# Kernel tuning notes

Hardware: AMD Instinct MI355X
Metric: run time of the kernel (lower is better)

The kernel has to match this reference:

```python
import jax, jax.numpy as jnp
import numpy as np

N_OSC = 256
N_LAYERS = 4
STEPS = 10
DT = 0.1
B = 1024
D_IN = 512
D_OUT = 128


def setup_inputs() -> dict:
    key = jax.random.key(0)
    ks = jax.random.split(key, 12)
    n = N_OSC

    def rn(k, shape, s=1.0):
        return jax.random.normal(k, shape, jnp.float32) * s

    K = rn(ks[0], (N_LAYERS, n, n), 0.1)
    K = (K + jnp.swapaxes(K, -1, -2)) / 2  # symmetric init as in torch
    return {
        "x": rn(ks[1], (B, D_IN)),
        "enc_W1": rn(ks[2], (D_IN, 2 * n), 0.02), "enc_b1": jnp.zeros((2 * n,), jnp.float32),
        "enc_W2": rn(ks[3], (2 * n, n), 0.02), "enc_b2": jnp.zeros((n,), jnp.float32),
        "K": K,
        "omega": rn(ks[4], (N_LAYERS, n), 0.1),
        "K_global": jnp.full((N_LAYERS,), 0.5, jnp.float32),
        "op_strength": jnp.full((6,), 0.5, jnp.float32),
        "exchange_logits": rn(ks[5], (n, n), 0.1),
        "catalyze_freq": rn(ks[6], (n,), 0.1),
        "sel_W1": rn(ks[7], (n + 2, 64), 0.05), "sel_b1": jnp.zeros((64,), jnp.float32),
        "sel_W2": rn(ks[8], (64, 6), 0.05), "sel_b2": jnp.zeros((6,), jnp.float32),
        "dec_W1": rn(ks[9], (2 * n, 2 * D_OUT), 0.02), "dec_b1": jnp.zeros((2 * D_OUT,), jnp.float32),
        "dec_W2": rn(ks[10], (2 * D_OUT, D_OUT), 0.02), "dec_b2": jnp.zeros((D_OUT,), jnp.float32),
        "z_momentum": jnp.float32(0.1),
        "z_decay": jnp.float32(0.05),
    }


def _kuramoto_layer(theta, K, omega, K_global):
    n = theta.shape[-1]

    def step(th, _):
        diff = th[:, None, :] - th[:, :, None]          # [B, i, j] = theta_j - theta_i
        coupling = jnp.sum(K * jnp.sin(diff), axis=-1)  # reduce over j -> [B, n]
        th_new = th + DT * (omega + (K_global / n) * coupling)
        th_new = jnp.arctan2(jnp.sin(th_new), jnp.cos(th_new))  # wrap to (-pi, pi]
        return th_new, None

    theta, _ = jax.lax.scan(jax.checkpoint(step), theta, None, length=STEPS)
    cm = jnp.mean(jnp.cos(theta), axis=-1)
    sm = jnp.mean(jnp.sin(theta), axis=-1)
    return theta, jnp.sqrt(cm * cm + sm * sm)  # Kuramoto order parameter r


def _soft_permutation(logits):
    P = logits
    for _ in range(5):  # Sinkhorn normalization in log space
        P = P - jax.nn.logsumexp(P, axis=-1, keepdims=True)
        P = P - jax.nn.logsumexp(P, axis=-2, keepdims=True)
    return jnp.exp(P)


def _forward(x, enc_W1, enc_b1, enc_W2, enc_b2, K, omega, K_global,
             op_strength, exchange_logits, catalyze_freq,
             sel_W1, sel_b1, sel_W2, sel_b2, dec_W1, dec_b1, dec_W2, dec_b2,
             z_momentum, z_decay):
    n = N_OSC
    # input encoding -> initial phases in (-pi, pi)
    h = jax.nn.gelu(x @ enc_W1 + enc_b1, approximate=False)
    theta = jnp.tanh(h @ enc_W2 + enc_b2) * jnp.pi

    z = jnp.float32(0.1)
    P = _soft_permutation(exchange_logits)
    k_mult = jnp.float32(1.0)              # AMPLIFY/CONTAIN carry to next layer
    om_add = jnp.zeros((n,), theta.dtype)  # CATALYZE carry to next layer

    for li in range(N_LAYERS):
        theta, r = _kuramoto_layer(theta, K[li] * k_mult, omega[li] + om_add, K_global[li])
        # z-coordinate attractor update: dz = mom*(r_mean - z) - decay*(z - 0.5)
        dz = z_momentum * (jnp.mean(r) - z) - z_decay * (z - 0.5)
        z = jnp.clip(z + 0.01 * dz, 0.0, 1.0)
        # APL operator selection from [theta, coherence, z]
        feat = jnp.concatenate(
            [theta, r[:, None], jnp.broadcast_to(z, (theta.shape[0], 1))], axis=-1)
        logits = jax.nn.gelu(feat @ sel_W1 + sel_b1, approximate=False) @ sel_W2 + sel_b2
        op = jnp.argmax(jnp.mean(logits, axis=0))
        strength = op_strength[op] * r[:, None]  # coherence-modulated strength
        sm_ = jnp.mean(strength)
        # apply operator: phase mods now, K/omega mods carried into next layer
        noise = jax.random.normal(jax.random.fold_in(jax.random.key(42), li),
                                  theta.shape, theta.dtype)
        theta = jnp.where(op == 3, theta @ P,                                # EXCHANGE
                          jnp.where(op == 4, theta + noise * strength * 0.2,  # INHIBIT
                                    theta))
        k_mult = jnp.where(op == 1, 1.0 + sm_ * 0.5,        # AMPLIFY
                           jnp.where(op == 2, 1.0 - sm_ * 0.3, 1.0))  # CONTAIN
        om_add = jnp.where(op == 5, catalyze_freq * sm_,    # CATALYZE
                           jnp.zeros_like(catalyze_freq))

    # decode from (cos, sin) phase embedding
    emb = jnp.concatenate([jnp.cos(theta), jnp.sin(theta)], axis=-1)  # [B, 2n]
    out = jax.nn.gelu(emb @ dec_W1 + dec_b1, approximate=False) @ dec_W2 + dec_b2
    return out


def reference(x, enc_W1, enc_b1, enc_W2, enc_b2, K, omega, K_global,
              op_strength, exchange_logits, catalyze_freq,
              sel_W1, sel_b1, sel_W2, sel_b2, dec_W1, dec_b1, dec_W2, dec_b2,
              z_momentum, z_decay):
    return _forward(x, enc_W1, enc_b1, enc_W2, enc_b2, K, omega, K_global,
                    op_strength, exchange_logits, catalyze_freq,
                    sel_W1, sel_b1, sel_W2, sel_b2, dec_W1, dec_b1, dec_W2, dec_b2,
                    z_momentum, z_decay)
```

## Files before the change

kernel.cpp:

```cpp
#include <hip/hip_runtime.h>
#include <hip/hip_fp16.h>
#include <math.h>

#define DT_F 0.1f

#define SC_Z     0
#define SC_RMEAN 1
#define SC_KMULT 2
#define SC_OP    3
#define SC_OPSTR 4
#define SC_SM    5

typedef __attribute__((ext_vector_type(8))) short short8;
typedef __attribute__((ext_vector_type(4))) float f32x4;


__device__ __forceinline__ float gelu_f(float x) {
    return 0.5f * x * (1.0f + erff(x * 0.7071067811865475f));
}

__device__ __forceinline__ unsigned short f2bf_rne(float f) {
    union { float f; unsigned u; } v; v.f = f;
    unsigned x = v.u;
    unsigned r = x + 0x7fffu + ((x >> 16) & 1u);
    return (unsigned short)(r >> 16);
}

__device__ __forceinline__ unsigned rotl32(unsigned v, int d) {
    return (v << d) | (v >> (32 - d));
}

__device__ __forceinline__ void threefry2x32(unsigned k0, unsigned k1,
                                             unsigned x0, unsigned x1,
                                             unsigned& o0, unsigned& o1) {
    unsigned k2 = k0 ^ k1 ^ 0x1BD11BDAu;
    x0 += k0; x1 += k1;
    const int r0[4] = {13, 15, 26, 6};
    const int r1[4] = {17, 29, 16, 24};
#pragma unroll
    for (int g = 0; g < 5; ++g) {
        const int* R = (g & 1) ? r1 : r0;
#pragma unroll
        for (int q = 0; q < 4; ++q) { x0 += x1; x1 = rotl32(x1, R[q]); x1 ^= x0; }
        unsigned a, b;
        switch (g) {
            case 0:  a = k1; b = k2 + 1u; break;
            case 1:  a = k2; b = k0 + 2u; break;
            case 2:  a = k0; b = k1 + 3u; break;
            case 3:  a = k1; b = k2 + 4u; break;
            default: a = k2; b = k0 + 5u; break;
        }
        x0 += a; x1 += b;
    }
    o0 = x0; o1 = x1;
}

__device__ __forceinline__ float erfinv_xla(float x) {
    float w = -log1pf(-x * x);
    float p;
    if (w < 5.0f) {
        w -= 2.5f;
        p = 2.81022636e-08f;
        p = fmaf(p, w, 3.43273939e-07f);
        p = fmaf(p, w, -3.5233877e-06f);
        p = fmaf(p, w, -4.39150654e-06f);
        p = fmaf(p, w, 0.00021858087f);
        p = fmaf(p, w, -0.00125372503f);
        p = fmaf(p, w, -0.00417768164f);
        p = fmaf(p, w, 0.246640727f);
        p = fmaf(p, w, 1.50140941f);
    } else {
        w = sqrtf(w) - 3.0f;
        p = -0.000200214257f;
        p = fmaf(p, w, 0.000100950558f);
        p = fmaf(p, w, 0.00134934322f);
        p = fmaf(p, w, -0.00367342844f);
        p = fmaf(p, w, 0.00573950773f);
        p = fmaf(p, w, -0.0076224613f);
        p = fmaf(p, w, 0.00943887047f);
        p = fmaf(p, w, 1.00167406f);
        p = fmaf(p, w, 2.83297682f);
    }
    return p * x;
}

__device__ __forceinline__ float jax_normal_elem(unsigned fk0, unsigned fk1, unsigned flat) {
    const unsigned HALF = 131072u;
    unsigned idx = (flat < HALF) ? flat : (flat - HALF);
    unsigned o0, o1;
    threefry2x32(fk0, fk1, idx, idx + HALF, o0, o1);
    unsigned bits = (flat < HALF) ? o0 : o1;
    float f = __uint_as_float((bits >> 9) | 0x3F800000u) - 1.0f;
    const float LO = __uint_as_float(0xBF7FFFFFu);
    float u = fmaxf(LO, fmaf(f, 2.0f, LO));
    return 1.41421356237f * erfinv_xla(u);
}


__global__ __launch_bounds__(256) void prep_wt_kernel(
    const float* __restrict__ W1, const float* __restrict__ W2,
    const float* __restrict__ W3, const float* __restrict__ W4,
    unsigned short* __restrict__ T1, unsigned short* __restrict__ T2,
    unsigned short* __restrict__ T3, unsigned short* __restrict__ T4)
{
    __shared__ float tile[64][65];
    int b = blockIdx.x;
    const float* W; unsigned short* T; int K, N, kt, nt;
    if (b < 64)       { W = W1; T = T1; K = 512; N = 512; kt = b >> 3; nt = b & 7; }
    else if (b < 96)  { b -= 64;  W = W2; T = T2; K = 512; N = 256; kt = b >> 2; nt = b & 3; }
    else if (b < 128) { b -= 96;  W = W3; T = T3; K = 512; N = 256; kt = b >> 2; nt = b & 3; }
    else              { b -= 128; W = W4; T = T4; K = 256; N = 128; kt = b >> 1; nt = b & 1; }
    const int k0 = kt * 64, n0 = nt * 64;
    const int t = threadIdx.x;

#pragma unroll
    for (int i = 0; i < 4; ++i) {
        int r = (t >> 4) + i * 16;
        int c = (t & 15) * 4;
        float4 v = *reinterpret_cast<const float4*>(&W[(k0 + r) * N + n0 + c]);
        tile[r][c] = v.x; tile[r][c + 1] = v.y; tile[r][c + 2] = v.z; tile[r][c + 3] = v.w;
    }
    __syncthreads();
#pragma unroll
    for (int i = 0; i < 4; ++i) {
        int nn = (t >> 4) + i * 16;
        int kc = (t & 15) * 4;
        ushort4 o;
        o.x = f2bf_rne(tile[kc + 0][nn]);
        o.y = f2bf_rne(tile[kc + 1][nn]);
        o.z = f2bf_rne(tile[kc + 2][nn]);
        o.w = f2bf_rne(tile[kc + 3][nn]);
        *reinterpret_cast<ushort4*>(&T[(n0 + nn) * K + k0 + kc]) = o;
    }
}


template <int ACT, int KF, bool EMB>
__global__ __launch_bounds__(256) void gemm_mfma_kernel(
    const float* __restrict__ A,
    const unsigned short* __restrict__ Wt,
    const float* __restrict__ bias,
    float* __restrict__ C, int N)
{
    constexpr int STR = KF + 8;
    __shared__ __align__(16) unsigned short A_s[64 * STR];
    __shared__ __align__(16) unsigned short B_s[64 * STR];
    const int tid = threadIdx.x;
    const int m_base = blockIdx.y * 64;
    const int n_base = blockIdx.x * 64;

    {
        constexpr int ITERS = 64 * KF / 2048;
#pragma unroll
        for (int c = 0; c < ITERS; ++c) {
            const int f = c * 2048 + tid * 8;
            const int row = f / KF, k = f % KF;
            float4 a0, a1;
            if (EMB) {
                const int kk = k & 255;
                a0 = *reinterpret_cast<const float4*>(&A[(m_base + row) * 256 + kk]);
                a1 = *reinterpret_cast<const float4*>(&A[(m_base + row) * 256 + kk + 4]);
                if (k < 256) {
                    a0.x = __cosf(a0.x); a0.y = __cosf(a0.y); a0.z = __cosf(a0.z); a0.w = __cosf(a0.w);
                    a1.x = __cosf(a1.x); a1.y = __cosf(a1.y); a1.z = __cosf(a1.z); a1.w = __cosf(a1.w);
                } else {
                    a0.x = __sinf(a0.x); a0.y = __sinf(a0.y); a0.z = __sinf(a0.z); a0.w = __sinf(a0.w);
                    a1.x = __sinf(a1.x); a1.y = __sinf(a1.y); a1.z = __sinf(a1.z); a1.w = __sinf(a1.w);
                }
            } else {
                a0 = *reinterpret_cast<const float4*>(&A[(m_base + row) * KF + k]);
                a1 = *reinterpret_cast<const float4*>(&A[(m_base + row) * KF + k + 4]);
            }
            short8 v;
            v[0] = (short)f2bf_rne(a0.x); v[1] = (short)f2bf_rne(a0.y);
            v[2] = (short)f2bf_rne(a0.z); v[3] = (short)f2bf_rne(a0.w);
            v[4] = (short)f2bf_rne(a1.x); v[5] = (short)f2bf_rne(a1.y);
            v[6] = (short)f2bf_rne(a1.z); v[7] = (short)f2bf_rne(a1.w);
            *reinterpret_cast<short8*>(&A_s[row * STR + k]) = v;
        }
    }
    {
        constexpr int ITERS = 64 * KF / 2048;
#pragma unroll
        for (int c = 0; c < ITERS; ++c) {
            const int f = c * 2048 + tid * 8;
            const int n = f / KF, k = f % KF;
            short8 v = *reinterpret_cast<const short8*>(&Wt[(n_base + n) * KF + k]);
            *reinterpret_cast<short8*>(&B_s[n * STR + k]) = v;
        }
    }
    __syncthreads();

    const int l = tid & 63, w = tid >> 6;
    const int lo = l & 15, hi = l >> 4;

    f32x4 acc0 = {0.f, 0.f, 0.f, 0.f};
    f32x4 acc1 = {0.f, 0.f, 0.f, 0.f};
    f32x4 acc2 = {0.f, 0.f, 0.f, 0.f};
    f32x4 acc3 = {0.f, 0.f, 0.f, 0.f};
#pragma unroll
    for (int kc = 0; kc < KF / 32; ++kc) {
        short8 af = *reinterpret_cast<const short8*>(&A_s[(w * 16 + lo) * STR + kc * 32 + hi * 8]);
        short8 b0 = *reinterpret_cast<const short8*>(&B_s[(0 * 16 + lo) * STR + kc * 32 + hi * 8]);
        short8 b1 = *reinterpret_cast<const short8*>(&B_s[(1 * 16 + lo) * STR + kc * 32 + hi * 8]);
        short8 b2 = *reinterpret_cast<const short8*>(&B_s[(2 * 16 + lo) * STR + kc * 32 + hi * 8]);
        short8 b3 = *reinterpret_cast<const short8*>(&B_s[(3 * 16 + lo) * STR + kc * 32 + hi * 8]);
        acc0 = __builtin_amdgcn_mfma_f32_16x16x32_bf16(af, b0, acc0, 0, 0, 0);
        acc1 = __builtin_amdgcn_mfma_f32_16x16x32_bf16(af, b1, acc1, 0, 0, 0);
        acc2 = __builtin_amdgcn_mfma_f32_16x16x32_bf16(af, b2, acc2, 0, 0, 0);
        acc3 = __builtin_amdgcn_mfma_f32_16x16x32_bf16(af, b3, acc3, 0, 0, 0);
    }

#pragma unroll
    for (int nf = 0; nf < 4; ++nf) {
        const f32x4 a = (nf == 0) ? acc0 : (nf == 1) ? acc1 : (nf == 2) ? acc2 : acc3;
        const int n = n_base + nf * 16 + lo;
        const float bv = bias[n];
#pragma unroll
        for (int q = 0; q < 4; ++q) {
            const int m = m_base + w * 16 + hi * 4 + q;
            float v = a[q] + bv;
            if (ACT == 1) v = gelu_f(v);
            else if (ACT == 2) v = tanhf(v) * 3.14159274101257324f;
            C[m * N + n] = v;
        }
    }
}


__global__ __launch_bounds__(1024) void sinkhorn_kernel(const float* __restrict__ logits,
                                                        float* __restrict__ P,
                                                        float* __restrict__ scal,
                                                        float* __restrict__ om_add) {
    __shared__ __align__(16) __half Eh[256][260];
    __shared__ float a[256], b[256];
    __shared__ float part[8][256];
    const int t = threadIdx.x;

    if (t < 8) {
        float val = 0.0f;
        if (t == SC_Z) val = 0.1f;
        if (t == SC_KMULT) val = 1.0f;
        scal[t] = val;
    }
    if (t < 256) { om_add[t] = 0.0f; b[t] = 1.0f; }

    {
        const int r = t >> 2, c0 = (t & 3) * 64;
#pragma unroll
        for (int j = 0; j < 64; j += 4) {
            float4 x4 = *reinterpret_cast<const float4*>(&logits[r * 256 + c0 + j]);
            __half2 h01 = __floats2half2_rn(__expf(x4.x), __expf(x4.y));
            __half2 h23 = __floats2half2_rn(__expf(x4.z), __expf(x4.w));
            *reinterpret_cast<__half2*>(&Eh[r][c0 + j])     = h01;
            *reinterpret_cast<__half2*>(&Eh[r][c0 + j + 2]) = h23;
        }
    }
    __syncthreads();

    for (int it = 0; it < 5; ++it) {
        {
            const int i = t & 255, q = t >> 8;
            float s0 = 0.f, s1 = 0.f, s2 = 0.f, s3 = 0.f;
#pragma unroll
            for (int j0 = 0; j0 < 64; j0 += 4) {
                float2 e4 = *reinterpret_cast<const float2*>(&Eh[i][q * 64 + j0]);
                const __half2* hp = reinterpret_cast<const __half2*>(&e4);
                float2 f01 = __half22float2(hp[0]);
                float2 f23 = __half22float2(hp[1]);
                float4 bv = *reinterpret_cast<const float4*>(&b[q * 64 + j0]);
                s0 = fmaf(f01.x, bv.x, s0);
                s1 = fmaf(f01.y, bv.y, s1);
                s2 = fmaf(f23.x, bv.z, s2);
                s3 = fmaf(f23.y, bv.w, s3);
            }
            part[q][i] = (s0 + s1) + (s2 + s3);
        }
        __syncthreads();
        if (t < 256) a[t] = 1.0f / (part[0][t] + part[1][t] + part[2][t] + part[3][t]);
        __syncthreads();
        {
            const int jp = t & 127, seg = t >> 7;
            float s0 = 0.f, s1 = 0.f;
#pragma unroll
            for (int i0 = 0; i0 < 32; i0 += 4) {
                float4 av = *reinterpret_cast<const float4*>(&a[seg * 32 + i0]);
                __half2 e0 = *reinterpret_cast<const __half2*>(&Eh[seg * 32 + i0 + 0][2 * jp]);
                __half2 e1 = *reinterpret_cast<const __half2*>(&Eh[seg * 32 + i0 + 1][2 * jp]);
                __half2 e2 = *reinterpret_cast<const __half2*>(&Eh[seg * 32 + i0 + 2][2 * jp]);
                __half2 e3 = *reinterpret_cast<const __half2*>(&Eh[seg * 32 + i0 + 3][2 * jp]);
                float2 f0 = __half22float2(e0), f1 = __half22float2(e1);
                float2 f2 = __half22float2(e2), f3 = __half22float2(e3);
                s0 = fmaf(f0.x, av.x, s0); s1 = fmaf(f0.y, av.x, s1);
                s0 = fmaf(f1.x, av.y, s0); s1 = fmaf(f1.y, av.y, s1);
                s0 = fmaf(f2.x, av.z, s0); s1 = fmaf(f2.y, av.z, s1);
                s0 = fmaf(f3.x, av.w, s0); s1 = fmaf(f3.y, av.w, s1);
            }
            part[seg][2 * jp]     = s0;
            part[seg][2 * jp + 1] = s1;
        }
        __syncthreads();
        if (t < 256) {
            float s = ((part[0][t] + part[1][t]) + (part[2][t] + part[3][t]))
                    + ((part[4][t] + part[5][t]) + (part[6][t] + part[7][t]));
            b[t] = 1.0f / s;
        }
        __syncthreads();
    }

    {
        const int r = t >> 2, c0 = (t & 3) * 64;
        const float ar = a[r];
#pragma unroll
        for (int j = 0; j < 64; j += 4) {
            float2 e4 = *reinterpret_cast<const float2*>(&Eh[r][c0 + j]);
            const __half2* hp = reinterpret_cast<const __half2*>(&e4);
            float2 f01 = __half22float2(hp[0]);
            float2 f23 = __half22float2(hp[1]);
            float4 bv = *reinterpret_cast<const float4*>(&b[c0 + j]);
            float4 o;
            o.x = f01.x * ar * bv.x;
            o.y = f01.y * ar * bv.y;
            o.z = f23.x * ar * bv.z;
            o.w = f23.y * ar * bv.w;
            *reinterpret_cast<float4*>(&P[r * 256 + c0 + j]) = o;
        }
    }
}


__global__ __launch_bounds__(512) void kuramoto_mfma_kernel(
    float* __restrict__ theta,
    const float* __restrict__ Kl,
    const float* __restrict__ omega_l,
    const float* __restrict__ Kg_p,
    const float* __restrict__ scal,
    const float* __restrict__ om_add,
    float* __restrict__ r_out,
    float* __restrict__ rpart,
    const float* __restrict__ P,
    int li)
{
    __shared__ __align__(16) unsigned short s_lds[2][16][264];
    __shared__ __align__(16) unsigned short c_lds[2][16][264];
    __shared__ __align__(16) float th_lds[16][260];
    __shared__ float rp_s[16][128];
    __shared__ float rp_c[16][128];
    __shared__ float red_s[16][32];
    __shared__ float red_c[16][32];
    __shared__ float rloc[16];

    const int tid = threadIdx.x;
    const int l  = tid & 63;
    const int w  = tid >> 6;
    const int lo = l & 15;
    const int hi = l >> 4;
    const int cb = w * 32;
    const int r0 = blockIdx.x * 16;

    const float gk = Kg_p[0] * (1.0f / 256.0f) * scal[SC_KMULT];
    const int op_prev = (int)scal[SC_OP];

    {
        const int row = tid >> 5;
        const int c0 = (tid & 31) * 8;
        float4 a = *reinterpret_cast<const float4*>(&theta[(r0 + row) * 256 + c0]);
        float4 b = *reinterpret_cast<const float4*>(&theta[(r0 + row) * 256 + c0 + 4]);
        *reinterpret_cast<float4*>(&th_lds[row][c0])     = a;
        *reinterpret_cast<float4*>(&th_lds[row][c0 + 4]) = b;
    }

    short8 kfrag[8][2];
#pragma unroll
    for (int nf = 0; nf < 2; ++nf) {
        const int col = cb + nf * 16 + lo;
        const float* krow = Kl + col * 256;
#pragma unroll
        for (int ks = 0; ks < 8; ++ks) {
            const int kb = ks * 32 + hi * 8;
            float4 k0 = *reinterpret_cast<const float4*>(&krow[kb]);
            float4 k1 = *reinterpret_cast<const float4*>(&krow[kb + 4]);
            short8 f;
            f[0] = (short)f2bf_rne(k0.x); f[1] = (short)f2bf_rne(k0.y);
            f[2] = (short)f2bf_rne(k0.z); f[3] = (short)f2bf_rne(k0.w);
            f[4] = (short)f2bf_rne(k1.x); f[5] = (short)f2bf_rne(k1.y);
            f[6] = (short)f2bf_rne(k1.z); f[7] = (short)f2bf_rne(k1.w);
            kfrag[ks][nf] = f;
        }
    }
    __syncthreads();

    float t[2][4];
    if (op_prev == 3) {
        float acc[2][4] = {};
        for (int j = 0; j < 256; ++j) {
            float p0 = P[j * 256 + cb + lo];
            float p1 = P[j * 256 + cb + 16 + lo];
#pragma unroll
            for (int q = 0; q < 4; ++q) {
                float tv = th_lds[hi * 4 + q][j];
                acc[0][q] = fmaf(tv, p0, acc[0][q]);
                acc[1][q] = fmaf(tv, p1, acc[1][q]);
            }
        }
#pragma unroll
        for (int nf = 0; nf < 2; ++nf)
#pragma unroll
            for (int q = 0; q < 4; ++q) t[nf][q] = acc[nf][q];
    } else {
#pragma unroll
        for (int nf = 0; nf < 2; ++nf)
#pragma unroll
            for (int q = 0; q < 4; ++q)
                t[nf][q] = th_lds[hi * 4 + q][cb + nf * 16 + lo];
        if (op_prev == 4) {
            unsigned fk0, fk1;
            threefry2x32(0u, 42u, 0u, (unsigned)(li - 1), fk0, fk1);
            const float opv = scal[SC_OPSTR];
#pragma unroll
            for (int nf = 0; nf < 2; ++nf)
#pragma unroll
                for (int q = 0; q < 4; ++q) {
                    const int row = hi * 4 + q;
                    const int col = cb + nf * 16 + lo;
                    unsigned flat = (unsigned)((r0 + row) * 256 + col);
                    float nz = jax_normal_elem(fk0, fk1, flat);
                    t[nf][q] += nz * opv * r_out[r0 + row] * 0.2f;
                }
        }
    }

    float si[2][4], ci[2][4];
    float om[2];
#pragma unroll
    for (int nf = 0; nf < 2; ++nf) {
        const int col = cb + nf * 16 + lo;
        om[nf] = omega_l[col] + om_add[col];
#pragma unroll
        for (int q = 0; q < 4; ++q) {
            const int row = hi * 4 + q;
            float sv, cv;
            __sincosf(t[nf][q], &sv, &cv);
            si[nf][q] = sv; ci[nf][q] = cv;
            s_lds[0][row][col] = f2bf_rne(sv);
            c_lds[0][row][col] = f2bf_rne(cv);
        }
    }
    __syncthreads();

    int cur = 0;
    for (int s = 0; s < 10; ++s) {
        f32x4 accS0 = {0.f, 0.f, 0.f, 0.f};
        f32x4 accS1 = {0.f, 0.f, 0.f, 0.f};
        f32x4 accC0 = {0.f, 0.f, 0.f, 0.f};
        f32x4 accC1 = {0.f, 0.f, 0.f, 0.f};
#pragma unroll
        for (int ks = 0; ks < 8; ++ks) {
            short8 aS = *reinterpret_cast<const short8*>(&s_lds[cur][lo][ks * 32 + hi * 8]);
            short8 aC = *reinterpret_cast<const short8*>(&c_lds[cur][lo][ks * 32 + hi * 8]);
            accS0 = __builtin_amdgcn_mfma_f32_16x16x32_bf16(aS, kfrag[ks][0], accS0, 0, 0, 0);
            accS1 = __builtin_amdgcn_mfma_f32_16x16x32_bf16(aS, kfrag[ks][1], accS1, 0, 0, 0);
            accC0 = __builtin_amdgcn_mfma_f32_16x16x32_bf16(aC, kfrag[ks][0], accC0, 0, 0, 0);
            accC1 = __builtin_amdgcn_mfma_f32_16x16x32_bf16(aC, kfrag[ks][1], accC1, 0, 0, 0);
        }
        const int nxt = cur ^ 1;
#pragma unroll
        for (int nf = 0; nf < 2; ++nf) {
#pragma unroll
            for (int q = 0; q < 4; ++q) {
                float aS = (nf == 0) ? accS0[q] : accS1[q];
                float aC = (nf == 0) ? accC0[q] : accC1[q];
                float coup = ci[nf][q] * aS - si[nf][q] * aC;
                float tn = t[nf][q] + DT_F * (om[nf] + gk * coup);
                t[nf][q] = tn;
                float sv, cv;
                __sincosf(tn, &sv, &cv);
                si[nf][q] = sv; ci[nf][q] = cv;
                const int row = hi * 4 + q;
                const int col = cb + nf * 16 + lo;
                s_lds[nxt][row][col] = f2bf_rne(sv);
                c_lds[nxt][row][col] = f2bf_rne(cv);
            }
        }
        __syncthreads();
        cur = nxt;
    }

#pragma unroll
    for (int q = 0; q < 4; ++q) {
        const int row = hi * 4 + q;
        rp_s[row][w * 16 + lo] = si[0][q] + si[1][q];
        rp_c[row][w * 16 + lo] = ci[0][q] + ci[1][q];
    }
#pragma unroll
    for (int nf = 0; nf < 2; ++nf) {
#pragma unroll
        for (int q = 0; q < 4; ++q) {
            const int row = hi * 4 + q;
            const int col = cb + nf * 16 + lo;
            theta[(r0 + row) * 256 + col] = atan2f(si[nf][q], ci[nf][q]);
        }
    }
    __syncthreads();

    {
        const int row = tid >> 5;
        const int i = tid & 31;
        float ssum = rp_s[row][i] + rp_s[row][i + 32] + rp_s[row][i + 64] + rp_s[row][i + 96];
        float csum = rp_c[row][i] + rp_c[row][i + 32] + rp_c[row][i + 64] + rp_c[row][i + 96];
        red_s[row][i] = ssum;
        red_c[row][i] = csum;
        __syncthreads();
#pragma unroll
        for (int off = 16; off > 0; off >>= 1) {
            if (i < off) {
                red_s[row][i] += red_s[row][i + off];
                red_c[row][i] += red_c[row][i + off];
            }
            __syncthreads();
        }
        if (i == 0) {
            float sm = red_s[row][0] * (1.0f / 256.0f);
            float cm = red_c[row][0] * (1.0f / 256.0f);
            float rv = sqrtf(cm * cm + sm * sm);
            r_out[r0 + row] = rv;
            rloc[row] = rv;
        }
        __syncthreads();
        if (tid == 0) {
            float s = 0.0f;
#pragma unroll
            for (int rr = 0; rr < 16; ++rr) s += rloc[rr];
            rpart[blockIdx.x] = s;
        }
    }
}


__global__ __launch_bounds__(256) void sel_partial_kernel(const float* __restrict__ theta,
                                                          const float* __restrict__ rbuf,
                                                          const float* __restrict__ rpart,
                                                          const float* __restrict__ scal,
                                                          const float* __restrict__ W1,
                                                          const float* __restrict__ b1,
                                                          const float* __restrict__ zm_p,
                                                          const float* __restrict__ zd_p,
                                                          float* __restrict__ partial) {
    __shared__ float Wt[64][261];
    __shared__ float th_s[4][256];
    __shared__ float gl[4][64];
    __shared__ float s_z;
    const int t = threadIdx.x;
    const int h = t & 63;
    const int rr = t >> 6;
    const int blk = blockIdx.x;

    if (t < 64) {
        float s = rpart[t];
#pragma unroll
        for (int off = 32; off > 0; off >>= 1) s += __shfl_down(s, off);
        if (t == 0) {
            float rmean = s * (1.0f / 1024.0f);
            float zp = scal[SC_Z];
            float dz = (*zm_p) * (rmean - zp) - (*zd_p) * (zp - 0.5f);
            float zn = zp + 0.01f * dz;
            s_z = fminf(fmaxf(zn, 0.0f), 1.0f);
        }
    }

    for (int idx = t; idx < 258 * 64; idx += 256)
        Wt[idx & 63][idx >> 6] = W1[idx];

    {
        const int c0 = h * 4;
        float4 v = *reinterpret_cast<const float4*>(&theta[(blk * 4 + rr) * 256 + c0]);
        *reinterpret_cast<float4*>(&th_s[rr][c0]) = v;
    }
    __syncthreads();

    const float z = s_z;
    float d0 = 0.f, d1 = 0.f, d2 = 0.f, d3 = 0.f;
#pragma unroll 4
    for (int k0 = 0; k0 < 256; k0 += 4) {
        float4 tv = *reinterpret_cast<const float4*>(&th_s[rr][k0]);
        d0 = fmaf(tv.x, Wt[h][k0 + 0], d0);
        d1 = fmaf(tv.y, Wt[h][k0 + 1], d1);
        d2 = fmaf(tv.z, Wt[h][k0 + 2], d2);
        d3 = fmaf(tv.w, Wt[h][k0 + 3], d3);
    }
    float full = (d0 + d1) + (d2 + d3) + b1[h]
               + rbuf[blk * 4 + rr] * Wt[h][256] + z * Wt[h][257];
    gl[rr][h] = gelu_f(full);
    __syncthreads();
    if (t < 64) partial[blk * 64 + t] = ((gl[0][t] + gl[1][t]) + gl[2][t]) + gl[3][t];
}


__global__ __launch_bounds__(256) void op_finalize_kernel(const float* __restrict__ partial,
                                                          const float* __restrict__ W2,
                                                          const float* __restrict__ b2,
                                                          const float* __restrict__ opstr,
                                                          const float* __restrict__ cf,
                                                          const float* __restrict__ rpart,
                                                          const float* __restrict__ zm_p,
                                                          const float* __restrict__ zd_p,
                                                          float* __restrict__ scal,
                                                          float* __restrict__ om_add) {
    __shared__ float red[4][64];
    __shared__ float hbar[64];
    __shared__ float lg[6];
    __shared__ float s_rmean;
    __shared__ float s_sm;
    __shared__ int s_op;
    const int t = threadIdx.x;
    const int h = t & 63;
    const int q = t >> 6;

    if (t < 64) {
        float s = rpart[t];
#pragma unroll
        for (int off = 32; off > 0; off >>= 1) s += __shfl_down(s, off);
        if (t == 0) s_rmean = s * (1.0f / 1024.0f);
    }

    float s = 0.0f;
#pragma unroll 8
    for (int blk = q * 64; blk < q * 64 + 64; ++blk) s += partial[blk * 64 + h];
    red[q][h] = s;
    __syncthreads();
    if (t < 64) hbar[t] = (red[0][t] + red[1][t] + red[2][t] + red[3][t]) * (1.0f / 1024.0f);
    __syncthreads();
    if (t < 6) {
        float l = b2[t];
        for (int hh = 0; hh < 64; ++hh) l = fmaf(hbar[hh], W2[hh * 6 + t], l);
        lg[t] = l;
    }
    __syncthreads();
    if (t == 0) {
        float rmean = s_rmean;
        float zp = scal[SC_Z];
        float dz = (*zm_p) * (rmean - zp) - (*zd_p) * (zp - 0.5f);
        float zn = zp + 0.01f * dz;
        zn = fminf(fmaxf(zn, 0.0f), 1.0f);
        scal[SC_Z] = zn;
        scal[SC_RMEAN] = rmean;

        float best = -1e30f;
        int op = 0;
#pragma unroll
        for (int o = 0; o < 6; ++o) {
            if (lg[o] > best) { best = lg[o]; op = o; }
        }
        float sm = opstr[op] * rmean;
        scal[SC_OP] = (float)op;
        scal[SC_OPSTR] = opstr[op];
        scal[SC_SM] = sm;
        scal[SC_KMULT] = (op == 1) ? (1.0f + sm * 0.5f)
                        : (op == 2) ? (1.0f - sm * 0.3f) : 1.0f;
        s_sm = sm;
        s_op = op;
    }
    __syncthreads();
    om_add[t] = (s_op == 5) ? cf[t] * s_sm : 0.0f;
}


__global__ __launch_bounds__(256) void apply_op_kernel(float* __restrict__ theta,
                                                       const float* __restrict__ P,
                                                       const float* __restrict__ r,
                                                       const float* __restrict__ scal,
                                                       int li) {
    __shared__ float th[8][256];
    const int op = (int)scal[SC_OP];
    const int i = threadIdx.x;
    const int b0 = blockIdx.x * 8;

    if (op == 3) {
#pragma unroll
        for (int rr = 0; rr < 8; ++rr) th[rr][i] = theta[(b0 + rr) * 256 + i];
        __syncthreads();
        float acc[8] = {0.f, 0.f, 0.f, 0.f, 0.f, 0.f, 0.f, 0.f};
        for (int j = 0; j < 256; ++j) {
            float pv = P[j * 256 + i];
#pragma unroll
            for (int rr = 0; rr < 8; ++rr) acc[rr] = fmaf(th[rr][j], pv, acc[rr]);
        }
#pragma unroll
        for (int rr = 0; rr < 8; ++rr) theta[(b0 + rr) * 256 + i] = acc[rr];
    } else if (op == 4) {
        unsigned fk0, fk1;
        threefry2x32(0u, 42u, 0u, (unsigned)li, fk0, fk1);
        const float opv = scal[SC_OPSTR];
#pragma unroll
        for (int rr = 0; rr < 8; ++rr) {
            int b = b0 + rr;
            unsigned flat = (unsigned)(b * 256 + i);
            float nz = jax_normal_elem(fk0, fk1, flat);
            float strength = opv * r[b];
            theta[b * 256 + i] += nz * strength * 0.2f;
        }
    }
}


extern "C" void kernel_launch(void* const* d_in, const int* in_sizes, int n_in,
                              void* d_out, int out_size, void* d_ws, size_t ws_size,
                              hipStream_t stream) {
    const float* x     = (const float*)d_in[0];
    const float* eW1   = (const float*)d_in[1];
    const float* eb1   = (const float*)d_in[2];
    const float* eW2   = (const float*)d_in[3];
    const float* eb2   = (const float*)d_in[4];
    const float* K     = (const float*)d_in[5];
    const float* omega = (const float*)d_in[6];
    const float* Kg    = (const float*)d_in[7];
    const float* opstr = (const float*)d_in[8];
    const float* exlog = (const float*)d_in[9];
    const float* cfreq = (const float*)d_in[10];
    const float* sW1   = (const float*)d_in[11];
    const float* sb1   = (const float*)d_in[12];
    const float* sW2   = (const float*)d_in[13];
    const float* sb2   = (const float*)d_in[14];
    const float* dW1   = (const float*)d_in[15];
    const float* db1   = (const float*)d_in[16];
    const float* dW2   = (const float*)d_in[17];
    const float* db2   = (const float*)d_in[18];
    const float* zm    = (const float*)d_in[19];
    const float* zd    = (const float*)d_in[20];
    float* out = (float*)d_out;

    float* ws      = (float*)d_ws;
    float* P       = ws;
    float* theta   = P + 65536;
    float* h       = theta + 262144;
    float* dh      = h + 524288;
    float* rbuf    = dh + 262144;
    float* scal    = rbuf + 1024;
    float* om_add  = scal + 8;
    float* partial = om_add + 256;
    float* rpart   = partial + 16384;
    unsigned short* W1t = (unsigned short*)(rpart + 64);
    unsigned short* W2t = (unsigned short*)(rpart + 64 + 131072);
    unsigned short* W3t = (unsigned short*)(rpart + 64 + 131072 + 65536);
    unsigned short* W4t = (unsigned short*)(rpart + 64 + 131072 + 65536 + 65536);

    prep_wt_kernel<<<136, 256, 0, stream>>>(eW1, eW2, dW1, dW2, W1t, W2t, W3t, W4t);
    sinkhorn_kernel<<<1, 1024, 0, stream>>>(exlog, P, scal, om_add);

    gemm_mfma_kernel<1, 512, false><<<dim3(8, 16), 256, 0, stream>>>(x, W1t, eb1, h, 512);
    gemm_mfma_kernel<2, 512, false><<<dim3(4, 16), 256, 0, stream>>>(h, W2t, eb2, theta, 256);

    for (int li = 0; li < 4; ++li) {
        kuramoto_mfma_kernel<<<64, 512, 0, stream>>>(theta, K + li * 65536, omega + li * 256,
                                                     Kg + li, scal, om_add, rbuf, rpart, P, li);
        sel_partial_kernel<<<256, 256, 0, stream>>>(theta, rbuf, rpart, scal, sW1, sb1,
                                                    zm, zd, partial);
        op_finalize_kernel<<<1, 256, 0, stream>>>(partial, sW2, sb2, opstr, cfreq, rpart,
                                                  zm, zd, scal, om_add);
    }

    apply_op_kernel<<<128, 256, 0, stream>>>(theta, P, rbuf, scal, 3);
    gemm_mfma_kernel<1, 512, true><<<dim3(4, 16), 256, 0, stream>>>(theta, W3t, db1, dh, 256);
    gemm_mfma_kernel<0, 256, false><<<dim3(2, 16), 256, 0, stream>>>(dh, W4t, db2, out, 128);

    (void)in_sizes; (void)n_in; (void)out_size; (void)ws_size;
}
```

Measured before the change: 204.9 us.

## Fuse all Kuramoto layers and selector into one cooperative persistent kernel

Replaces the per-layer sequence of kuramoto, selector-partial and op-finalize kernels, plus the final apply-op kernel, with one cooperative kernel of 64 blocks. Blocks keep theta in LDS across layers and use grid.sync for the global reductions. This is meant to remove about 13 kernel launches and the theta round-trips through global memory between them. In exchange it adds three grid-wide barriers per layer, and the selector work now runs on only 64 blocks instead of 256. It also relies on volatile reads of scal and om_add for cross-block visibility.

```diff
diff --git a/kernel.cpp b/kernel.cpp
--- a/kernel.cpp
+++ b/kernel.cpp
@@ -1,6 +1,9 @@
 #include <hip/hip_runtime.h>
+#include <hip/hip_cooperative_groups.h>
 #include <hip/hip_fp16.h>
 #include <math.h>
+
+namespace cg = cooperative_groups;
 
 #define DT_F 0.1f
 
@@ -329,18 +332,27 @@
 }
 
 
-__global__ __launch_bounds__(512) void kuramoto_mfma_kernel(
-    float* __restrict__ theta,
-    const float* __restrict__ Kl,
-    const float* __restrict__ omega_l,
-    const float* __restrict__ Kg_p,
-    const float* __restrict__ scal,
-    const float* __restrict__ om_add,
-    float* __restrict__ r_out,
-    float* __restrict__ rpart,
-    const float* __restrict__ P,
-    int li)
+__global__ __launch_bounds__(512) void mega_layers_kernel(
+    float* theta,
+    const float* Kall,
+    const float* omega,
+    const float* Kg,
+    const float* opstr,
+    const float* cf,
+    const float* sW1,
+    const float* sb1,
+    const float* sW2,
+    const float* sb2,
+    const float* zm_p,
+    const float* zd_p,
+    float* scal,
+    float* om_add,
+    float* rpart,
+    float* partial,
+    const float* P)
 {
+    cg::grid_group grid = cg::this_grid();
+
     __shared__ __align__(16) unsigned short s_lds[2][16][264];
     __shared__ __align__(16) unsigned short c_lds[2][16][264];
     __shared__ __align__(16) float th_lds[16][260];
@@ -349,6 +361,11 @@
     __shared__ float red_s[16][32];
     __shared__ float red_c[16][32];
     __shared__ float rloc[16];
+    __shared__ float red8[8][64];
+    __shared__ float hbar[64];
+    __shared__ float lg[6];
+    __shared__ float s_z, s_rmean, s_sm;
+    __shared__ int s_op;
 
     const int tid = threadIdx.x;
     const int l  = tid & 63;
@@ -358,9 +375,6 @@
     const int cb = w * 32;
     const int r0 = blockIdx.x * 16;
 
-    const float gk = Kg_p[0] * (1.0f / 256.0f) * scal[SC_KMULT];
-    const int op_prev = (int)scal[SC_OP];
-
     {
         const int row = tid >> 5;
         const int c0 = (tid & 31) * 8;
@@ -369,336 +383,318 @@
         *reinterpret_cast<float4*>(&th_lds[row][c0])     = a;
         *reinterpret_cast<float4*>(&th_lds[row][c0 + 4]) = b;
     }
-
-    short8 kfrag[8][2];
-#pragma unroll
-    for (int nf = 0; nf < 2; ++nf) {
-        const int col = cb + nf * 16 + lo;
-        const float* krow = Kl + col * 256;
-#pragma unroll
-        for (int ks = 0; ks < 8; ++ks) {
-            const int kb = ks * 32 + hi * 8;
-            float4 k0 = *reinterpret_cast<const float4*>(&krow[kb]);
-            float4 k1 = *reinterpret_cast<const float4*>(&krow[kb + 4]);
-            short8 f;
-            f[0] = (short)f2bf_rne(k0.x); f[1] = (short)f2bf_rne(k0.y);
-            f[2] = (short)f2bf_rne(k0.z); f[3] = (short)f2bf_rne(k0.w);
-            f[4] = (short)f2bf_rne(k1.x); f[5] = (short)f2bf_rne(k1.y);
-            f[6] = (short)f2bf_rne(k1.z); f[7] = (short)f2bf_rne(k1.w);
-            kfrag[ks][nf] = f;
-        }
-    }
     __syncthreads();
 
-    float t[2][4];
-    if (op_prev == 3) {
-        float acc[2][4] = {};
-        for (int j = 0; j < 256; ++j) {
-            float p0 = P[j * 256 + cb + lo];
-            float p1 = P[j * 256 + cb + 16 + lo];
+    for (int li = 0; li < 4; ++li) {
+        const float* Kl = Kall + li * 65536;
+        short8 kfrag[8][2];
+#pragma unroll
+        for (int nf = 0; nf < 2; ++nf) {
+            const int col = cb + nf * 16 + lo;
+            const float* krow = Kl + col * 256;
+#pragma unroll
+            for (int ks = 0; ks < 8; ++ks) {
+                const int kb = ks * 32 + hi * 8;
+                float4 k0 = *reinterpret_cast<const float4*>(&krow[kb]);
+                float4 k1 = *reinterpret_cast<const float4*>(&krow[kb + 4]);
+                short8 f;
+                f[0] = (short)f2bf_rne(k0.x); f[1] = (short)f2bf_rne(k0.y);
+                f[2] = (short)f2bf_rne(k0.z); f[3] = (short)f2bf_rne(k0.w);
+                f[4] = (short)f2bf_rne(k1.x); f[5] = (short)f2bf_rne(k1.y);
+                f[6] = (short)f2bf_rne(k1.z); f[7] = (short)f2bf_rne(k1.w);
+                kfrag[ks][nf] = f;
+            }
+        }
+
+        const int op_prev = (li == 0) ? 0 : (int)*(volatile float*)(scal + SC_OP);
+        const float kmult = (li == 0) ? 1.0f : *(volatile float*)(scal + SC_KMULT);
+        const float opv_p = (li == 0) ? 0.0f : *(volatile float*)(scal + SC_OPSTR);
+        const float gk = Kg[li] * (1.0f / 256.0f) * kmult;
+
+        float t[2][4];
+        if (op_prev == 3) {
+            float acc[2][4] = {};
+            for (int j = 0; j < 256; ++j) {
+                float p0 = P[j * 256 + cb + lo];
+                float p1 = P[j * 256 + cb + 16 + lo];
+#pragma unroll
+                for (int q = 0; q < 4; ++q) {
+                    float tv = th_lds[hi * 4 + q][j];
+                    acc[0][q] = fmaf(tv, p0, acc[0][q]);
+                    acc[1][q] = fmaf(tv, p1, acc[1][q]);
+                }
+            }
+#pragma unroll
+            for (int nf = 0; nf < 2; ++nf)
+#pragma unroll
+                for (int q = 0; q < 4; ++q) t[nf][q] = acc[nf][q];
+        } else {
+#pragma unroll
+            for (int nf = 0; nf < 2; ++nf)
+#pragma unroll
+                for (int q = 0; q < 4; ++q)
+                    t[nf][q] = th_lds[hi * 4 + q][cb + nf * 16 + lo];
+            if (op_prev == 4) {
+                unsigned fk0, fk1;
+                threefry2x32(0u, 42u, 0u, (unsigned)(li - 1), fk0, fk1);
+#pragma unroll
+                for (int nf = 0; nf < 2; ++nf)
+#pragma unroll
+                    for (int q = 0; q < 4; ++q) {
+                        const int row = hi * 4 + q;
+                        const int col = cb + nf * 16 + lo;
+                        unsigned flat = (unsigned)((r0 + row) * 256 + col);
+                        float nz = jax_normal_elem(fk0, fk1, flat);
+                        t[nf][q] += nz * opv_p * rloc[row] * 0.2f;
+                    }
+            }
+        }
+
+        float si[2][4], ci[2][4];
+        float om[2];
+#pragma unroll
+        for (int nf = 0; nf < 2; ++nf) {
+            const int col = cb + nf * 16 + lo;
+            om[nf] = omega[li * 256 + col]
+                   + ((li == 0) ? 0.0f : *(volatile float*)(om_add + col));
 #pragma unroll
             for (int q = 0; q < 4; ++q) {
-                float tv = th_lds[hi * 4 + q][j];
-                acc[0][q] = fmaf(tv, p0, acc[0][q]);
-                acc[1][q] = fmaf(tv, p1, acc[1][q]);
-            }
-        }
-#pragma unroll
-        for (int nf = 0; nf < 2; ++nf)
-#pragma unroll
-            for (int q = 0; q < 4; ++q) t[nf][q] = acc[nf][q];
-    } else {
-#pragma unroll
-        for (int nf = 0; nf < 2; ++nf)
-#pragma unroll
-            for (int q = 0; q < 4; ++q)
-                t[nf][q] = th_lds[hi * 4 + q][cb + nf * 16 + lo];
-        if (op_prev == 4) {
-            unsigned fk0, fk1;
-            threefry2x32(0u, 42u, 0u, (unsigned)(li - 1), fk0, fk1);
-            const float opv = scal[SC_OPSTR];
-#pragma unroll
-            for (int nf = 0; nf < 2; ++nf)
+                const int row = hi * 4 + q;
+                float sv, cv;
+                __sincosf(t[nf][q], &sv, &cv);
+                si[nf][q] = sv; ci[nf][q] = cv;
+                s_lds[0][row][col] = f2bf_rne(sv);
+                c_lds[0][row][col] = f2bf_rne(cv);
+            }
+        }
+        __syncthreads();
+
+        int cur = 0;
+        for (int s = 0; s < 10; ++s) {
+            f32x4 accS0 = {0.f, 0.f, 0.f, 0.f};
+            f32x4 accS1 = {0.f, 0.f, 0.f, 0.f};
+            f32x4 accC0 = {0.f, 0.f, 0.f, 0.f};
+            f32x4 accC1 = {0.f, 0.f, 0.f, 0.f};
+#pragma unroll
+            for (int ks = 0; ks < 8; ++ks) {
+                short8 aS = *reinterpret_cast<const short8*>(&s_lds[cur][lo][ks * 32 + hi * 8]);
+                short8 aC = *reinterpret_cast<const short8*>(&c_lds[cur][lo][ks * 32 + hi * 8]);
+                accS0 = __builtin_amdgcn_mfma_f32_16x16x32_bf16(aS, kfrag[ks][0], accS0, 0, 0, 0);
+                accS1 = __builtin_amdgcn_mfma_f32_16x16x32_bf16(aS, kfrag[ks][1], accS1, 0, 0, 0);
+                accC0 = __builtin_amdgcn_mfma_f32_16x16x32_bf16(aC, kfrag[ks][0], accC0, 0, 0, 0);
+                accC1 = __builtin_amdgcn_mfma_f32_16x16x32_bf16(aC, kfrag[ks][1], accC1, 0, 0, 0);
+            }
+            const int nxt = cur ^ 1;
+#pragma unroll
+            for (int nf = 0; nf < 2; ++nf) {
 #pragma unroll
                 for (int q = 0; q < 4; ++q) {
+                    float aS = (nf == 0) ? accS0[q] : accS1[q];
+                    float aC = (nf == 0) ? accC0[q] : accC1[q];
+                    float coup = ci[nf][q] * aS - si[nf][q] * aC;
+                    float tn = t[nf][q] + DT_F * (om[nf] + gk * coup);
+                    t[nf][q] = tn;
+                    float sv, cv;
+                    __sincosf(tn, &sv, &cv);
+                    si[nf][q] = sv; ci[nf][q] = cv;
                     const int row = hi * 4 + q;
                     const int col = cb + nf * 16 + lo;
-                    unsigned flat = (unsigned)((r0 + row) * 256 + col);
-                    float nz = jax_normal_elem(fk0, fk1, flat);
-                    t[nf][q] += nz * opv * r_out[r0 + row] * 0.2f;
+                    s_lds[nxt][row][col] = f2bf_rne(sv);
+                    c_lds[nxt][row][col] = f2bf_rne(cv);
                 }
-        }
-    }
-
-    float si[2][4], ci[2][4];
-    float om[2];
-#pragma unroll
-    for (int nf = 0; nf < 2; ++nf) {
-        const int col = cb + nf * 16 + lo;
-        om[nf] = omega_l[col] + om_add[col];
+            }
+            __syncthreads();
+            cur = nxt;
+        }
+
 #pragma unroll
         for (int q = 0; q < 4; ++q) {
             const int row = hi * 4 + q;
-            float sv, cv;
-            __sincosf(t[nf][q], &sv, &cv);
-            si[nf][q] = sv; ci[nf][q] = cv;
-            s_lds[0][row][col] = f2bf_rne(sv);
-            c_lds[0][row][col] = f2bf_rne(cv);
-        }
-    }
-    __syncthreads();
-
-    int cur = 0;
-    for (int s = 0; s < 10; ++s) {
-        f32x4 accS0 = {0.f, 0.f, 0.f, 0.f};
-        f32x4 accS1 = {0.f, 0.f, 0.f, 0.f};
-        f32x4 accC0 = {0.f, 0.f, 0.f, 0.f};
-        f32x4 accC1 = {0.f, 0.f, 0.f, 0.f};
-#pragma unroll
-        for (int ks = 0; ks < 8; ++ks) {
-            short8 aS = *reinterpret_cast<const short8*>(&s_lds[cur][lo][ks * 32 + hi * 8]);
-            short8 aC = *reinterpret_cast<const short8*>(&c_lds[cur][lo][ks * 32 + hi * 8]);
-            accS0 = __builtin_amdgcn_mfma_f32_16x16x32_bf16(aS, kfrag[ks][0], accS0, 0, 0, 0);
-            accS1 = __builtin_amdgcn_mfma_f32_16x16x32_bf16(aS, kfrag[ks][1], accS1, 0, 0, 0);
-            accC0 = __builtin_amdgcn_mfma_f32_16x16x32_bf16(aC, kfrag[ks][0], accC0, 0, 0, 0);
-            accC1 = __builtin_amdgcn_mfma_f32_16x16x32_bf16(aC, kfrag[ks][1], accC1, 0, 0, 0);
-        }
-        const int nxt = cur ^ 1;
+            rp_s[row][w * 16 + lo] = si[0][q] + si[1][q];
+            rp_c[row][w * 16 + lo] = ci[0][q] + ci[1][q];
+        }
 #pragma unroll
         for (int nf = 0; nf < 2; ++nf) {
 #pragma unroll
             for (int q = 0; q < 4; ++q) {
-                float aS = (nf == 0) ? accS0[q] : accS1[q];
-                float aC = (nf == 0) ? accC0[q] : accC1[q];
-                float coup = ci[nf][q] * aS - si[nf][q] * aC;
-                float tn = t[nf][q] + DT_F * (om[nf] + gk * coup);
-                t[nf][q] = tn;
-                float sv, cv;
-                __sincosf(tn, &sv, &cv);
-                si[nf][q] = sv; ci[nf][q] = cv;
                 const int row = hi * 4 + q;
                 const int col = cb + nf * 16 + lo;
-                s_lds[nxt][row][col] = f2bf_rne(sv);
-                c_lds[nxt][row][col] = f2bf_rne(cv);
+                th_lds[row][col] = atan2f(si[nf][q], ci[nf][q]);
             }
         }
         __syncthreads();
-        cur = nxt;
-    }
-
-#pragma unroll
-    for (int q = 0; q < 4; ++q) {
-        const int row = hi * 4 + q;
-        rp_s[row][w * 16 + lo] = si[0][q] + si[1][q];
-        rp_c[row][w * 16 + lo] = ci[0][q] + ci[1][q];
-    }
-#pragma unroll
-    for (int nf = 0; nf < 2; ++nf) {
-#pragma unroll
-        for (int q = 0; q < 4; ++q) {
-            const int row = hi * 4 + q;
-            const int col = cb + nf * 16 + lo;
-            theta[(r0 + row) * 256 + col] = atan2f(si[nf][q], ci[nf][q]);
-        }
-    }
-    __syncthreads();
+        {
+            const int row = tid >> 5;
+            const int i = tid & 31;
+            float ssum = rp_s[row][i] + rp_s[row][i + 32] + rp_s[row][i + 64] + rp_s[row][i + 96];
+            float csum = rp_c[row][i] + rp_c[row][i + 32] + rp_c[row][i + 64] + rp_c[row][i + 96];
+            red_s[row][i] = ssum;
+            red_c[row][i] = csum;
+            __syncthreads();
+#pragma unroll
+            for (int off = 16; off > 0; off >>= 1) {
+                if (i < off) {
+                    red_s[row][i] += red_s[row][i + off];
+                    red_c[row][i] += red_c[row][i + off];
+                }
+                __syncthreads();
+            }
+            if (i == 0) {
+                float sm = red_s[row][0] * (1.0f / 256.0f);
+                float cm = red_c[row][0] * (1.0f / 256.0f);
+                rloc[row] = sqrtf(cm * cm + sm * sm);
+            }
+            __syncthreads();
+            if (tid == 0) {
+                float s = 0.0f;
+#pragma unroll
+                for (int rr = 0; rr < 16; ++rr) s += rloc[rr];
+                rpart[blockIdx.x] = s;
+            }
+        }
+        __threadfence();
+        grid.sync();
+
+        if (tid < 64) {
+            float s = *(volatile float*)(rpart + tid);
+#pragma unroll
+            for (int off = 32; off > 0; off >>= 1) s += __shfl_down(s, off);
+            if (tid == 0) {
+                float rmean = s * (1.0f / 1024.0f);
+                s_rmean = rmean;
+                float zp = *(volatile float*)(scal + SC_Z);
+                float dz = (*zm_p) * (rmean - zp) - (*zd_p) * (zp - 0.5f);
+                float zn = zp + 0.01f * dz;
+                s_z = fminf(fmaxf(zn, 0.0f), 1.0f);
+            }
+        }
+        __syncthreads();
+
+        {
+            const int h = tid & 63;
+            const int g = tid >> 6;
+            const int rA = g * 2, rB = g * 2 + 1;
+            const float z = s_z;
+            float a0 = 0.f, a1 = 0.f, b0 = 0.f, b1 = 0.f;
+#pragma unroll 4
+            for (int k = 0; k < 256; k += 2) {
+                float w0 = sW1[k * 64 + h];
+                float w1 = sW1[(k + 1) * 64 + h];
+                a0 = fmaf(th_lds[rA][k],     w0, a0);
+                a1 = fmaf(th_lds[rA][k + 1], w1, a1);
+                b0 = fmaf(th_lds[rB][k],     w0, b0);
+                b1 = fmaf(th_lds[rB][k + 1], w1, b1);
+            }
+            const float w256 = sW1[256 * 64 + h];
+            const float w257 = sW1[257 * 64 + h];
+            const float bb = sb1[h];
+            float fullA = a0 + a1 + bb + rloc[rA] * w256 + z * w257;
+            float fullB = b0 + b1 + bb + rloc[rB] * w256 + z * w257;
+            red8[g][h] = gelu_f(fullA) + gelu_f(fullB);
+        }
+        __syncthreads();
+        if (tid < 64) {
+            float s = ((red8[0][tid] + red8[1][tid]) + (red8[2][tid] + red8[3][tid]))
+                    + ((red8[4][tid] + red8[5][tid]) + (red8[6][tid] + red8[7][tid]));
+            partial[blockIdx.x * 64 + tid] = s;
+        }
+        __threadfence();
+        grid.sync();
+
+        if (blockIdx.x == 0) {
+            const int h = tid & 63;
+            const int q = tid >> 6;
+            float s = 0.0f;
+#pragma unroll
+            for (int bb = q * 8; bb < q * 8 + 8; ++bb)
+                s += *(volatile float*)(partial + bb * 64 + h);
+            red8[q][h] = s;
+            __syncthreads();
+            if (tid < 64)
+                hbar[tid] = (((red8[0][tid] + red8[1][tid]) + (red8[2][tid] + red8[3][tid]))
+                           + ((red8[4][tid] + red8[5][tid]) + (red8[6][tid] + red8[7][tid])))
+                          * (1.0f / 1024.0f);
+            __syncthreads();
+            if (tid < 6) {
+                float lv = sb2[tid];
+                for (int hh = 0; hh < 64; ++hh) lv = fmaf(hbar[hh], sW2[hh * 6 + tid], lv);
+                lg[tid] = lv;
+            }
+            __syncthreads();
+            if (tid == 0) {
+                scal[SC_Z] = s_z;
+                scal[SC_RMEAN] = s_rmean;
+                float best = -1e30f;
+                int op = 0;
+#pragma unroll
+                for (int o = 0; o < 6; ++o) {
+                    if (lg[o] > best) { best = lg[o]; op = o; }
+                }
+                float sm = opstr[op] * s_rmean;
+                scal[SC_OP] = (float)op;
+                scal[SC_OPSTR] = opstr[op];
+                scal[SC_SM] = sm;
+                scal[SC_KMULT] = (op == 1) ? (1.0f + sm * 0.5f)
+                                : (op == 2) ? (1.0f - sm * 0.3f) : 1.0f;
+                s_sm = sm;
+                s_op = op;
+            }
+            __syncthreads();
+            if (tid < 256) om_add[tid] = (s_op == 5) ? cf[tid] * s_sm : 0.0f;
+        }
+        __threadfence();
+        grid.sync();
+    }
 
     {
-        const int row = tid >> 5;
-        const int i = tid & 31;
-        float ssum = rp_s[row][i] + rp_s[row][i + 32] + rp_s[row][i + 64] + rp_s[row][i + 96];
-        float csum = rp_c[row][i] + rp_c[row][i + 32] + rp_c[row][i + 64] + rp_c[row][i + 96];
-        red_s[row][i] = ssum;
-        red_c[row][i] = csum;
-        __syncthreads();
-#pragma unroll
-        for (int off = 16; off > 0; off >>= 1) {
-            if (i < off) {
-                red_s[row][i] += red_s[row][i + off];
-                red_c[row][i] += red_c[row][i + off];
-            }
-            __syncthreads();
-        }
-        if (i == 0) {
-            float sm = red_s[row][0] * (1.0f / 256.0f);
-            float cm = red_c[row][0] * (1.0f / 256.0f);
-            float rv = sqrtf(cm * cm + sm * sm);
-            r_out[r0 + row] = rv;
-            rloc[row] = rv;
-        }
-        __syncthreads();
-        if (tid == 0) {
-            float s = 0.0f;
-#pragma unroll
-            for (int rr = 0; rr < 16; ++rr) s += rloc[rr];
-            rpart[blockIdx.x] = s;
-        }
-    }
-}
-
-
-__global__ __launch_bounds__(256) void sel_partial_kernel(const float* __restrict__ theta,
-                                                          const float* __restrict__ rbuf,
-                                                          const float* __restrict__ rpart,
-                                                          const float* __restrict__ scal,
-                                                          const float* __restrict__ W1,
-                                                          const float* __restrict__ b1,
-                                                          const float* __restrict__ zm_p,
-                                                          const float* __restrict__ zd_p,
-                                                          float* __restrict__ partial) {
-    __shared__ float Wt[64][261];
-    __shared__ float th_s[4][256];
-    __shared__ float gl[4][64];
-    __shared__ float s_z;
-    const int t = threadIdx.x;
-    const int h = t & 63;
-    const int rr = t >> 6;
-    const int blk = blockIdx.x;
-
-    if (t < 64) {
-        float s = rpart[t];
-#pragma unroll
-        for (int off = 32; off > 0; off >>= 1) s += __shfl_down(s, off);
-        if (t == 0) {
-            float rmean = s * (1.0f / 1024.0f);
-            float zp = scal[SC_Z];
-            float dz = (*zm_p) * (rmean - zp) - (*zd_p) * (zp - 0.5f);
-            float zn = zp + 0.01f * dz;
-            s_z = fminf(fmaxf(zn, 0.0f), 1.0f);
-        }
-    }
-
-    for (int idx = t; idx < 258 * 64; idx += 256)
-        Wt[idx & 63][idx >> 6] = W1[idx];
-
-    {
-        const int c0 = h * 4;
-        float4 v = *reinterpret_cast<const float4*>(&theta[(blk * 4 + rr) * 256 + c0]);
-        *reinterpret_cast<float4*>(&th_s[rr][c0]) = v;
-    }
-    __syncthreads();
-
-    const float z = s_z;
-    float d0 = 0.f, d1 = 0.f, d2 = 0.f, d3 = 0.f;
-#pragma unroll 4
-    for (int k0 = 0; k0 < 256; k0 += 4) {
-        float4 tv = *reinterpret_cast<const float4*>(&th_s[rr][k0]);
-        d0 = fmaf(tv.x, Wt[h][k0 + 0], d0);
-        d1 = fmaf(tv.y, Wt[h][k0 + 1], d1);
-        d2 = fmaf(tv.z, Wt[h][k0 + 2], d2);
-        d3 = fmaf(tv.w, Wt[h][k0 + 3], d3);
-    }
-    float full = (d0 + d1) + (d2 + d3) + b1[h]
-               + rbuf[blk * 4 + rr] * Wt[h][256] + z * Wt[h][257];
-    gl[rr][h] = gelu_f(full);
-    __syncthreads();
-    if (t < 64) partial[blk * 64 + t] = ((gl[0][t] + gl[1][t]) + gl[2][t]) + gl[3][t];
-}
-
-
-__global__ __launch_bounds__(256) void op_finalize_kernel(const float* __restrict__ partial,
-                                                          const float* __restrict__ W2,
-                                                          const float* __restrict__ b2,
-                                                          const float* __restrict__ opstr,
-                                                          const float* __restrict__ cf,
-                                                          const float* __restrict__ rpart,
-                                                          const float* __restrict__ zm_p,
-                                                          const float* __restrict__ zd_p,
-                                                          float* __restrict__ scal,
-                                                          float* __restrict__ om_add) {
-    __shared__ float red[4][64];
-    __shared__ float hbar[64];
-    __shared__ float lg[6];
-    __shared__ float s_rmean;
-    __shared__ float s_sm;
-    __shared__ int s_op;
-    const int t = threadIdx.x;
-    const int h = t & 63;
-    const int q = t >> 6;
-
-    if (t < 64) {
-        float s = rpart[t];
-#pragma unroll
-        for (int off = 32; off > 0; off >>= 1) s += __shfl_down(s, off);
-        if (t == 0) s_rmean = s * (1.0f / 1024.0f);
-    }
-
-    float s = 0.0f;
-#pragma unroll 8
-    for (int blk = q * 64; blk < q * 64 + 64; ++blk) s += partial[blk * 64 + h];
-    red[q][h] = s;
-    __syncthreads();
-    if (t < 64) hbar[t] = (red[0][t] + red[1][t] + red[2][t] + red[3][t]) * (1.0f / 1024.0f);
-    __syncthreads();
-    if (t < 6) {
-        float l = b2[t];
-        for (int hh = 0; hh < 64; ++hh) l = fmaf(hbar[hh], W2[hh * 6 + t], l);
-        lg[t] = l;
-    }
-    __syncthreads();
-    if (t == 0) {
-        float rmean = s_rmean;
-        float zp = scal[SC_Z];
-        float dz = (*zm_p) * (rmean - zp) - (*zd_p) * (zp - 0.5f);
-        float zn = zp + 0.01f * dz;
-        zn = fminf(fmaxf(zn, 0.0f), 1.0f);
-        scal[SC_Z] = zn;
-        scal[SC_RMEAN] = rmean;
-
-        float best = -1e30f;
-        int op = 0;
-#pragma unroll
-        for (int o = 0; o < 6; ++o) {
-            if (lg[o] > best) { best = lg[o]; op = o; }
-        }
-        float sm = opstr[op] * rmean;
-        scal[SC_OP] = (float)op;
-        scal[SC_OPSTR] = opstr[op];
-        scal[SC_SM] = sm;
-        scal[SC_KMULT] = (op == 1) ? (1.0f + sm * 0.5f)
-                        : (op == 2) ? (1.0f - sm * 0.3f) : 1.0f;
-        s_sm = sm;
-        s_op = op;
-    }
-    __syncthreads();
-    om_add[t] = (s_op == 5) ? cf[t] * s_sm : 0.0f;
-}
-
-
-__global__ __launch_bounds__(256) void apply_op_kernel(float* __restrict__ theta,
-                                                       const float* __restrict__ P,
-                                                       const float* __restrict__ r,
-                                                       const float* __restrict__ scal,
-                                                       int li) {
-    __shared__ float th[8][256];
-    const int op = (int)scal[SC_OP];
-    const int i = threadIdx.x;
-    const int b0 = blockIdx.x * 8;
-
-    if (op == 3) {
-#pragma unroll
-        for (int rr = 0; rr < 8; ++rr) th[rr][i] = theta[(b0 + rr) * 256 + i];
-        __syncthreads();
-        float acc[8] = {0.f, 0.f, 0.f, 0.f, 0.f, 0.f, 0.f, 0.f};
-        for (int j = 0; j < 256; ++j) {
-            float pv = P[j * 256 + i];
-#pragma unroll
-            for (int rr = 0; rr < 8; ++rr) acc[rr] = fmaf(th[rr][j], pv, acc[rr]);
-        }
-#pragma unroll
-        for (int rr = 0; rr < 8; ++rr) theta[(b0 + rr) * 256 + i] = acc[rr];
-    } else if (op == 4) {
-        unsigned fk0, fk1;
-        threefry2x32(0u, 42u, 0u, (unsigned)li, fk0, fk1);
-        const float opv = scal[SC_OPSTR];
-#pragma unroll
-        for (int rr = 0; rr < 8; ++rr) {
-            int b = b0 + rr;
-            unsigned flat = (unsigned)(b * 256 + i);
-            float nz = jax_normal_elem(fk0, fk1, flat);
-            float strength = opv * r[b];
-            theta[b * 256 + i] += nz * strength * 0.2f;
-        }
+        const int op = (int)*(volatile float*)(scal + SC_OP);
+        const float opv = *(volatile float*)(scal + SC_OPSTR);
+        float t[2][4];
+        if (op == 3) {
+            float acc[2][4] = {};
+            for (int j = 0; j < 256; ++j) {
+                float p0 = P[j * 256 + cb + lo];
+                float p1 = P[j * 256 + cb + 16 + lo];
+#pragma unroll
+                for (int q = 0; q < 4; ++q) {
+                    float tv = th_lds[hi * 4 + q][j];
+                    acc[0][q] = fmaf(tv, p0, acc[0][q]);
+                    acc[1][q] = fmaf(tv, p1, acc[1][q]);
+                }
+            }
+#pragma unroll
+            for (int nf = 0; nf < 2; ++nf)
+#pragma unroll
+                for (int q = 0; q < 4; ++q) t[nf][q] = acc[nf][q];
+        } else {
+#pragma unroll
+            for (int nf = 0; nf < 2; ++nf)
+#pragma unroll
+                for (int q = 0; q < 4; ++q)
+                    t[nf][q] = th_lds[hi * 4 + q][cb + nf * 16 + lo];
+            if (op == 4) {
+                unsigned fk0, fk1;
+                threefry2x32(0u, 42u, 0u, 3u, fk0, fk1);
+#pragma unroll
+                for (int nf = 0; nf < 2; ++nf)
+#pragma unroll
+                    for (int q = 0; q < 4; ++q) {
+                        const int row = hi * 4 + q;
+                        const int col = cb + nf * 16 + lo;
+                        unsigned flat = (unsigned)((r0 + row) * 256 + col);
+                        float nz = jax_normal_elem(fk0, fk1, flat);
+                        t[nf][q] += nz * opv * rloc[row] * 0.2f;
+                    }
+            }
+        }
+#pragma unroll
+        for (int nf = 0; nf < 2; ++nf)
+#pragma unroll
+            for (int q = 0; q < 4; ++q) {
+                const int row = hi * 4 + q;
+                const int col = cb + nf * 16 + lo;
+                theta[(r0 + row) * 256 + col] = t[nf][q];
+            }
     }
 }
 
@@ -750,16 +746,18 @@
     gemm_mfma_kernel<1, 512, false><<<dim3(8, 16), 256, 0, stream>>>(x, W1t, eb1, h, 512);
     gemm_mfma_kernel<2, 512, false><<<dim3(4, 16), 256, 0, stream>>>(h, W2t, eb2, theta, 256);
 
-    for (int li = 0; li < 4; ++li) {
-        kuramoto_mfma_kernel<<<64, 512, 0, stream>>>(theta, K + li * 65536, omega + li * 256,
-                                                     Kg + li, scal, om_add, rbuf, rpart, P, li);
-        sel_partial_kernel<<<256, 256, 0, stream>>>(theta, rbuf, rpart, scal, sW1, sb1,
-                                                    zm, zd, partial);
-        op_finalize_kernel<<<1, 256, 0, stream>>>(partial, sW2, sb2, opstr, cfreq, rpart,
-                                                  zm, zd, scal, om_add);
-    }
-
-    apply_op_kernel<<<128, 256, 0, stream>>>(theta, P, rbuf, scal, 3);
+    {
+        void* args[] = {
+            (void*)&theta, (void*)&K, (void*)&omega, (void*)&Kg,
+            (void*)&opstr, (void*)&cfreq, (void*)&sW1, (void*)&sb1,
+            (void*)&sW2, (void*)&sb2, (void*)&zm, (void*)&zd,
+            (void*)&scal, (void*)&om_add, (void*)&rpart, (void*)&partial,
+            (void*)&P
+        };
+        hipLaunchCooperativeKernel(mega_layers_kernel, dim3(64), dim3(512),
+                                   args, 0, stream);
+    }
+
     gemm_mfma_kernel<1, 512, true><<<dim3(4, 16), 256, 0, stream>>>(theta, W3t, db1, dh, 256);
     gemm_mfma_kernel<0, 256, false><<<dim3(2, 16), 256, 0, stream>>>(dh, W4t, db2, out, 128);
 
```

Result: slower. 425.4 us (+107.7%).
